# Kernel tuning notes

Measured on AMD Instinct MI355X. Metric: run time of the kernel, lower is better.

Reference implementation:

```python
import jax, jax.numpy as jnp
import numpy as np

B, N, D, C, H = 32, 36, 2048, 4, 512  # batch, regions, feat dim, coord dim, fusion hidden


def setup_inputs() -> dict:
    key = jax.random.key(0)
    ks = jax.random.split(key, 8)
    w = lambda k, sh: jax.random.normal(k, sh, dtype=jnp.float32) * 0.02
    return {
        "mm": jax.random.normal(ks[0], (B, N, D), dtype=jnp.float32),
        "coords": jax.random.uniform(ks[1], (B, N, C), dtype=jnp.float32),
        # MLB fusion params for coords: z = (x@W_cl * y@W_cr) @ W_cout
        "W_cl": w(ks[2], (C, H)),
        "W_cr": w(ks[3], (C, H)),
        "W_cout": w(ks[4], (H, D)),
        # MLB fusion params for features
        "W_fl": w(ks[5], (D, H)),
        "W_fr": w(ks[6], (D, H)),
        "W_fout": w(ks[7], (H, D)),
    }


def reference(mm, coords, W_cl, W_cr, W_cout, W_fl, W_fr, W_fout):
    # Project once per region (avoids projecting inside the N*N expand).
    cl = coords @ W_cl            # [B,N,H]
    cr = coords @ W_cr            # [B,N,H]
    fl = mm @ W_fl                # [B,N,H]
    fr = mm @ W_fr                # [B,N,H]
    # All-pairs bilinear fusion: Rij = f_coord(c_i, c_j) + f_feat(m_i, m_j)
    pair_c = cl[:, :, None, :] * cr[:, None, :, :]   # [B,N,N,H]
    pair_f = fl[:, :, None, :] * fr[:, None, :, :]   # [B,N,N,H]
    Rij = (jnp.einsum('bijh,hd->bijd', pair_c, W_cout)
           + jnp.einsum('bijh,hd->bijd', pair_f, W_fout))  # [B,N,N,D]
    # agg['type'] == 'max': reduce over the right (j) region axis
    mm_new = Rij.max(axis=2)      # [B,N,D]
    # residual
    return mm_new + mm
```

## Files before the change

kernel.cpp:

```cpp
#include <hip/hip_runtime.h>


typedef __attribute__((ext_vector_type(8))) short short8;
typedef __attribute__((ext_vector_type(4))) short short4v;
typedef __attribute__((ext_vector_type(4))) float f32x4;

__device__ __forceinline__ float bf2f(unsigned short h) {
  return __uint_as_float(((unsigned int)h) << 16);
}
__device__ __forceinline__ unsigned short f2bf(float f) {
  unsigned int u = __float_as_uint(f);
  u += 0x7FFFu + ((u >> 16) & 1u);
  return (unsigned short)(u >> 16);
}
__device__ __forceinline__ void gl2lds16(const void* g, void* l) {
  __builtin_amdgcn_global_load_lds(
      (const __attribute__((address_space(1))) unsigned int*)g,
      (__attribute__((address_space(3))) unsigned int*)l, 16, 0, 0);
}

__global__ __launch_bounds__(256) void k_prep(
    const float* __restrict__ coords, const float* __restrict__ Wcl,
    const float* __restrict__ Wcr, const float* __restrict__ mm,
    const float* __restrict__ Wcout, const float* __restrict__ Wfout,
    const float* __restrict__ Wfl, const float* __restrict__ Wfr,
    unsigned short* __restrict__ Lw, unsigned short* __restrict__ Rw,
    unsigned short* __restrict__ mmb, unsigned short* __restrict__ WS,
    unsigned short* __restrict__ WS2) {
  const int bid = blockIdx.x;
  if (bid < 2304) {
    int idx = bid * 256 + threadIdx.x;
    int row = idx >> 9, h = idx & 511;
    const float* c = coords + row * 4;
    float a0 = c[0], a1 = c[1], a2 = c[2], a3 = c[3];
    float vl = a0 * Wcl[h] + a1 * Wcl[512 + h] + a2 * Wcl[1024 + h] + a3 * Wcl[1536 + h];
    float vr = a0 * Wcr[h] + a1 * Wcr[512 + h] + a2 * Wcr[1024 + h] + a3 * Wcr[1536 + h];
    Lw[(size_t)row * 1024 + h] = f2bf(vl);
    Rw[(size_t)row * 1024 + h] = f2bf(vr);
    float4 m4 = *(const float4*)(mm + (size_t)row * 2048 + h * 4);
    short4v o;
    o[0] = (short)f2bf(m4.x); o[1] = (short)f2bf(m4.y);
    o[2] = (short)f2bf(m4.z); o[3] = (short)f2bf(m4.w);
    *(short4v*)(mmb + (size_t)row * 2048 + h * 4) = o;
  } else {
    int gi = (bid - 2304) * 256 + threadIdx.x;
    if (gi < 262144) {
      int n = gi & 15, qv = (gi >> 4) & 3, kc = (gi >> 6) & 31, g2 = gi >> 11;
      int d = g2 * 16 + n;
      int kbase = kc * 32 + qv * 8;
      const float* src = (kbase < 512) ? (Wcout + (size_t)kbase * 2048 + d)
                                       : (Wfout + (size_t)(kbase - 512) * 2048 + d);
      short8 o;
#pragma unroll
      for (int e = 0; e < 8; ++e) o[e] = (short)f2bf(src[(size_t)e * 2048]);
      *(short8*)(WS + (size_t)gi * 8) = o;
    } else {
      int gj = gi - 262144;
      int n = gj & 15, qv = (gj >> 4) & 3, kc = (gj >> 6) & 63, cg = gj >> 12;
      int col = cg * 16 + n;
      int dbase = kc * 32 + qv * 8;
      const float* src = (col < 512) ? (Wfl + (size_t)dbase * 512 + col)
                                     : (Wfr + (size_t)dbase * 512 + (col - 512));
      short8 o;
#pragma unroll
      for (int e = 0; e < 8; ++e) o[e] = (short)f2bf(src[(size_t)e * 512]);
      *(short8*)(WS2 + (size_t)gj * 8) = o;
    }
  }
}

__global__ __launch_bounds__(256) void k_proj_feat(
    const unsigned short* __restrict__ mmb, const unsigned short* __restrict__ WS2,
    unsigned short* __restrict__ Lw, unsigned short* __restrict__ Rw) {
  const int tid = threadIdx.x;
  const int lane = tid & 63, w = tid >> 6;
  const int n = lane & 15, q = lane >> 4;
  const int m0 = blockIdx.y * 16;
  const int cg = blockIdx.x * 4 + w;
  const int c0 = cg * 16;

  f32x4 acc = {0.f, 0.f, 0.f, 0.f};
#pragma unroll 4
  for (int kc = 0; kc < 64; ++kc) {
    short8 a = *(const short8*)(mmb + (size_t)(m0 + n) * 2048 + kc * 32 + q * 8);
    short8 b = *(const short8*)(WS2 + (size_t)(cg * 64 + kc) * 512 + lane * 8);
    acc = __builtin_amdgcn_mfma_f32_16x16x32_bf16(a, b, acc, 0, 0, 0);
  }
#pragma unroll
  for (int e = 0; e < 4; ++e) {
    int row = m0 + q * 4 + e;
    int col = c0 + n;
    unsigned short v = f2bf(acc[e]);
    if (col < 512) Lw[(size_t)row * 1024 + 512 + col] = v;
    else           Rw[(size_t)row * 1024 + col] = v;
  }
}

__global__ __launch_bounds__(256) void k_prod(
    const unsigned short* __restrict__ Lw, const unsigned short* __restrict__ Rw,
    unsigned short* __restrict__ Pf) {
  int idx = blockIdx.x * 256 + threadIdx.x;
  int lane = idx & 63;
  int gran = idx >> 6;
  int qg = gran / 288;
  int rem = gran - qg * 288;
  int kc = rem / 9;
  int t = rem - kc * 9;
  int n = lane & 15, q = lane >> 4;
  int k0 = kc * 32 + q * 8;
  int b = qg / 9;
  int g, j;
  if (t < 8) { g = qg * 4 + (t >> 1); j = (t & 1) * 16 + n; }
  else       { g = qg * 4 + (n >> 2); j = 32 + (n & 3); }
  short8 cl8 = *(const short8*)(Lw + (size_t)g * 1024 + k0);
  short8 cr8 = *(const short8*)(Rw + (size_t)(b * 36 + j) * 1024 + k0);
  short8 p;
#pragma unroll
  for (int e = 0; e < 8; ++e)
    p[e] = (short)f2bf(bf2f((unsigned short)cl8[e]) * bf2f((unsigned short)cr8[e]));
  *(short8*)(Pf + (size_t)idx * 8) = p;
}

__global__ __launch_bounds__(512, 2) void k_pairwise(
    const unsigned short* __restrict__ Pf, const unsigned short* __restrict__ WS,
    const float* __restrict__ mm, float* __restrict__ out) {
  __shared__ __align__(16) unsigned short lB[2][9 * 512];

  const int tid = threadIdx.x;
  const int lane = tid & 63, w = tid >> 6;
  const int n = lane & 15, q = lane >> 4;
  const int bx = blockIdx.x;
  const int dt = bx & 7, qg = bx >> 3;
  const int g0 = qg * 4;

  f32x4 acc[9][2];
#pragma unroll
  for (int t = 0; t < 9; ++t)
#pragma unroll
    for (int r = 0; r < 2; ++r) acc[t][r] = (f32x4){0.f, 0.f, 0.f, 0.f};

  const unsigned short* Abase = WS + ((size_t)(dt * 16 + w * 2) * 32) * 512 + lane * 8;
  const unsigned short* Bbase = Pf + (size_t)qg * 32 * 9 * 512;

  short8 aR[2], aN[2];
  gl2lds16(Bbase + (size_t)w * 512 + lane * 8, &lB[0][w * 512]);
  if (w == 0) gl2lds16(Bbase + (size_t)8 * 512 + lane * 8, &lB[0][8 * 512]);
  aR[0] = *(const short8*)(Abase);
  aR[1] = *(const short8*)(Abase + 32 * 512);
  __syncthreads();

#pragma unroll 2
  for (int kc = 0; kc < 32; ++kc) {
    const int buf = kc & 1;
    if (kc < 31) {
      const unsigned short* bn = Bbase + (size_t)((kc + 1) * 9) * 512 + lane * 8;
      gl2lds16(bn + (size_t)w * 512, &lB[buf ^ 1][w * 512]);
      if (w == 0) gl2lds16(bn + (size_t)8 * 512, &lB[buf ^ 1][8 * 512]);
      aN[0] = *(const short8*)(Abase + (size_t)(kc + 1) * 512);
      aN[1] = *(const short8*)(Abase + (size_t)(32 + kc + 1) * 512);
    }
    short8 bb[9];
#pragma unroll
    for (int t = 0; t < 9; ++t)
      bb[t] = *(const short8*)(&lB[buf][t * 512 + lane * 8]);
#pragma unroll
    for (int t = 0; t < 9; ++t) {
      acc[t][0] = __builtin_amdgcn_mfma_f32_16x16x32_bf16(aR[0], bb[t], acc[t][0], 0, 0, 0);
      acc[t][1] = __builtin_amdgcn_mfma_f32_16x16x32_bf16(aR[1], bb[t], acc[t][1], 0, 0, 0);
    }
    __syncthreads();
    aR[0] = aN[0];
    aR[1] = aN[1];
  }

#pragma unroll
  for (int r = 0; r < 2; ++r) {
#pragma unroll
    for (int e = 0; e < 4; ++e) {
      float vs = acc[8][r][e];
#pragma unroll
      for (int ii = 0; ii < 4; ++ii) {
        float v = fmaxf(acc[ii * 2][r][e], acc[ii * 2 + 1][r][e]);
        v = fmaxf(v, ((n >> 2) == ii) ? vs : -1e30f);
#pragma unroll
        for (int s = 1; s < 16; s <<= 1) v = fmaxf(v, __shfl_xor(v, s, 64));
        if (n == 0) {
          int d = dt * 256 + w * 32 + r * 16 + q * 4 + e;
          size_t o = (size_t)(g0 + ii) * 2048 + d;
          out[o] = v + mm[o];
        }
      }
    }
  }
}

extern "C" void kernel_launch(void* const* d_in, const int* in_sizes, int n_in,
                              void* d_out, int out_size, void* d_ws, size_t ws_size,
                              hipStream_t stream) {
  const float* mm     = (const float*)d_in[0];
  const float* coords = (const float*)d_in[1];
  const float* Wcl    = (const float*)d_in[2];
  const float* Wcr    = (const float*)d_in[3];
  const float* Wcout  = (const float*)d_in[4];
  const float* Wfl    = (const float*)d_in[5];
  const float* Wfr    = (const float*)d_in[6];
  const float* Wfout  = (const float*)d_in[7];
  float* out = (float*)d_out;

  unsigned short* Lw  = (unsigned short*)d_ws;
  unsigned short* Rw  = Lw + 1152 * 1024;
  unsigned short* WS  = Rw + 1152 * 1024;
  unsigned short* WS2 = WS + (size_t)262144 * 8;
  unsigned short* mmb = WS2 + (size_t)262144 * 8;
  unsigned short* Pf  = mmb + (size_t)1152 * 2048;

  k_prep<<<2304 + 2048, 256, 0, stream>>>(coords, Wcl, Wcr, mm, Wcout, Wfout,
                                          Wfl, Wfr, Lw, Rw, mmb, WS, WS2);
  k_proj_feat<<<dim3(16, 72), 256, 0, stream>>>(mmb, WS2, Lw, Rw);
  k_prod<<<20736, 256, 0, stream>>>(Lw, Rw, Pf);
  k_pairwise<<<2304, 512, 0, stream>>>(Pf, WS, mm, out);
}
```

Before: 338.7 us.

## Fuse pairwise product formation into the MFMA kernel, dropping the Pf buffer

Removes the separate k_prod kernel that materialized the bf16 pairwise products into a large global buffer. k_pairwise now loads Lw/Rw rows per k-chunk into registers, multiplies them and writes the products into the LDS double buffer one stage ahead. This replaces global_load_lds copies. It avoids a large global write and the repeated reads across the eight d-tiles, at the cost of recomputing the products per d-tile and adding VALU work and register pressure inside the main loop.

```diff
diff --git a/kernel.cpp b/kernel.cpp
--- a/kernel.cpp
+++ b/kernel.cpp
@@ -12,11 +12,6 @@
   unsigned int u = __float_as_uint(f);
   u += 0x7FFFu + ((u >> 16) & 1u);
   return (unsigned short)(u >> 16);
-}
-__device__ __forceinline__ void gl2lds16(const void* g, void* l) {
-  __builtin_amdgcn_global_load_lds(
-      (const __attribute__((address_space(1))) unsigned int*)g,
-      (__attribute__((address_space(3))) unsigned int*)l, 16, 0, 0);
 }
 
 __global__ __launch_bounds__(256) void k_prep(
@@ -96,34 +91,10 @@
   }
 }
 
-__global__ __launch_bounds__(256) void k_prod(
+__global__ __launch_bounds__(512, 2) void k_pairwise(
     const unsigned short* __restrict__ Lw, const unsigned short* __restrict__ Rw,
-    unsigned short* __restrict__ Pf) {
-  int idx = blockIdx.x * 256 + threadIdx.x;
-  int lane = idx & 63;
-  int gran = idx >> 6;
-  int qg = gran / 288;
-  int rem = gran - qg * 288;
-  int kc = rem / 9;
-  int t = rem - kc * 9;
-  int n = lane & 15, q = lane >> 4;
-  int k0 = kc * 32 + q * 8;
-  int b = qg / 9;
-  int g, j;
-  if (t < 8) { g = qg * 4 + (t >> 1); j = (t & 1) * 16 + n; }
-  else       { g = qg * 4 + (n >> 2); j = 32 + (n & 3); }
-  short8 cl8 = *(const short8*)(Lw + (size_t)g * 1024 + k0);
-  short8 cr8 = *(const short8*)(Rw + (size_t)(b * 36 + j) * 1024 + k0);
-  short8 p;
-#pragma unroll
-  for (int e = 0; e < 8; ++e)
-    p[e] = (short)f2bf(bf2f((unsigned short)cl8[e]) * bf2f((unsigned short)cr8[e]));
-  *(short8*)(Pf + (size_t)idx * 8) = p;
-}
-
-__global__ __launch_bounds__(512, 2) void k_pairwise(
-    const unsigned short* __restrict__ Pf, const unsigned short* __restrict__ WS,
-    const float* __restrict__ mm, float* __restrict__ out) {
+    const unsigned short* __restrict__ WS, const float* __restrict__ mm,
+    float* __restrict__ out) {
   __shared__ __align__(16) unsigned short lB[2][9 * 512];
 
   const int tid = threadIdx.x;
@@ -132,6 +103,48 @@
   const int bx = blockIdx.x;
   const int dt = bx & 7, qg = bx >> 3;
   const int g0 = qg * 4;
+  const int b = qg / 9;
+
+  const int tA = tid >> 6, lsA = tid & 63, nA = lsA & 15, qA = lsA >> 4;
+  const int gA = g0 + (tA >> 1);
+  const int jA = (tA & 1) * 16 + nA;
+  const unsigned short* clA = Lw + (size_t)gA * 1024 + qA * 8;
+  const unsigned short* crA = Rw + (size_t)(b * 36 + jA) * 1024 + qA * 8;
+  const int offA = tA * 512 + lsA * 8;
+  const bool hasB = (tid < 64);
+  const int nB = tid & 15, qB = (tid >> 4) & 3;
+  const int gB = g0 + (nB >> 2);
+  const int jB = 32 + (nB & 3);
+  const unsigned short* clB = Lw + (size_t)gB * 1024 + qB * 8;
+  const unsigned short* crB = Rw + (size_t)(b * 36 + jB) * 1024 + qB * 8;
+  const int offB = 8 * 512 + tid * 8;
+
+  short8 sclA, scrA, sclB, scrB;
+#define SLOAD(kc_)                                                   \
+  do {                                                               \
+    sclA = *(const short8*)(clA + (kc_) * 32);                       \
+    scrA = *(const short8*)(crA + (kc_) * 32);                       \
+    if (hasB) {                                                      \
+      sclB = *(const short8*)(clB + (kc_) * 32);                     \
+      scrB = *(const short8*)(crB + (kc_) * 32);                     \
+    }                                                                \
+  } while (0)
+
+#define SFIN(buf_)                                                   \
+  do {                                                               \
+    short8 p;                                                        \
+    _Pragma("unroll") for (int e = 0; e < 8; ++e)                    \
+        p[e] = (short)f2bf(bf2f((unsigned short)sclA[e]) *           \
+                           bf2f((unsigned short)scrA[e]));           \
+    *(short8*)(&lB[buf_][offA]) = p;                                 \
+    if (hasB) {                                                      \
+      short8 pb;                                                     \
+      _Pragma("unroll") for (int e = 0; e < 8; ++e)                  \
+          pb[e] = (short)f2bf(bf2f((unsigned short)sclB[e]) *        \
+                              bf2f((unsigned short)scrB[e]));        \
+      *(short8*)(&lB[buf_][offB]) = pb;                              \
+    }                                                                \
+  } while (0)
 
   f32x4 acc[9][2];
 #pragma unroll
@@ -140,11 +153,10 @@
     for (int r = 0; r < 2; ++r) acc[t][r] = (f32x4){0.f, 0.f, 0.f, 0.f};
 
   const unsigned short* Abase = WS + ((size_t)(dt * 16 + w * 2) * 32) * 512 + lane * 8;
-  const unsigned short* Bbase = Pf + (size_t)qg * 32 * 9 * 512;
-
   short8 aR[2], aN[2];
-  gl2lds16(Bbase + (size_t)w * 512 + lane * 8, &lB[0][w * 512]);
-  if (w == 0) gl2lds16(Bbase + (size_t)8 * 512 + lane * 8, &lB[0][8 * 512]);
+
+  SLOAD(0);
+  SFIN(0);
   aR[0] = *(const short8*)(Abase);
   aR[1] = *(const short8*)(Abase + 32 * 512);
   __syncthreads();
@@ -153,9 +165,7 @@
   for (int kc = 0; kc < 32; ++kc) {
     const int buf = kc & 1;
     if (kc < 31) {
-      const unsigned short* bn = Bbase + (size_t)((kc + 1) * 9) * 512 + lane * 8;
-      gl2lds16(bn + (size_t)w * 512, &lB[buf ^ 1][w * 512]);
-      if (w == 0) gl2lds16(bn + (size_t)8 * 512, &lB[buf ^ 1][8 * 512]);
+      SLOAD(kc + 1);
       aN[0] = *(const short8*)(Abase + (size_t)(kc + 1) * 512);
       aN[1] = *(const short8*)(Abase + (size_t)(32 + kc + 1) * 512);
     }
@@ -168,10 +178,13 @@
       acc[t][0] = __builtin_amdgcn_mfma_f32_16x16x32_bf16(aR[0], bb[t], acc[t][0], 0, 0, 0);
       acc[t][1] = __builtin_amdgcn_mfma_f32_16x16x32_bf16(aR[1], bb[t], acc[t][1], 0, 0, 0);
     }
+    if (kc < 31) SFIN(buf ^ 1);
     __syncthreads();
     aR[0] = aN[0];
     aR[1] = aN[1];
   }
+#undef SLOAD
+#undef SFIN
 
 #pragma unroll
   for (int r = 0; r < 2; ++r) {
@@ -212,11 +225,9 @@
   unsigned short* WS  = Rw + 1152 * 1024;
   unsigned short* WS2 = WS + (size_t)262144 * 8;
   unsigned short* mmb = WS2 + (size_t)262144 * 8;
-  unsigned short* Pf  = mmb + (size_t)1152 * 2048;
 
   k_prep<<<2304 + 2048, 256, 0, stream>>>(coords, Wcl, Wcr, mm, Wcout, Wfout,
                                           Wfl, Wfr, Lw, Rw, mmb, WS, WS2);
   k_proj_feat<<<dim3(16, 72), 256, 0, stream>>>(mmb, WS2, Lw, Rw);
-  k_prod<<<20736, 256, 0, stream>>>(Lw, Rw, Pf);
-  k_pairwise<<<2304, 512, 0, stream>>>(Pf, WS, mm, out);
-}
+  k_pairwise<<<2304, 512, 0, stream>>>(Lw, Rw, WS, mm, out);
+}
```

New measurement: 442.6 us. 1.31x slower.

## Halve pairwise block to 4 waves, each computing 4 D-tiles, reorder grid dt-major

Applied to the files above, without the earlier changes.

The pairwise GEMM block shrinks from 8 to 4 waves, and each wave now accumulates 4 output 16-row tiles instead of 2. This doubles register-level reuse of each LDS B fragment per wave and halves the per-block LDS load work per MFMA. The block index mapping is swapped so consecutive blocks share the same weight slice dt while varying qg, which changes L2 locality for the weight operand. Accumulator register pressure doubles (36 f32x4 tiles), and the unroll-2 pragma is dropped, which may reduce occupancy or cause spills.

```diff
diff --git a/kernel.cpp b/kernel.cpp
--- a/kernel.cpp
+++ b/kernel.cpp
@@ -121,7 +121,7 @@
   *(short8*)(Pf + (size_t)idx * 8) = p;
 }
 
-__global__ __launch_bounds__(512, 2) void k_pairwise(
+__global__ __launch_bounds__(256, 2) void k_pairwise(
     const unsigned short* __restrict__ Pf, const unsigned short* __restrict__ WS,
     const float* __restrict__ mm, float* __restrict__ out) {
   __shared__ __align__(16) unsigned short lB[2][9 * 512];
@@ -130,51 +130,54 @@
   const int lane = tid & 63, w = tid >> 6;
   const int n = lane & 15, q = lane >> 4;
   const int bx = blockIdx.x;
-  const int dt = bx & 7, qg = bx >> 3;
+  const int dt = bx / 288, qg = bx % 288;
   const int g0 = qg * 4;
 
-  f32x4 acc[9][2];
+  f32x4 acc[9][4];
 #pragma unroll
   for (int t = 0; t < 9; ++t)
 #pragma unroll
-    for (int r = 0; r < 2; ++r) acc[t][r] = (f32x4){0.f, 0.f, 0.f, 0.f};
-
-  const unsigned short* Abase = WS + ((size_t)(dt * 16 + w * 2) * 32) * 512 + lane * 8;
+    for (int r = 0; r < 4; ++r) acc[t][r] = (f32x4){0.f, 0.f, 0.f, 0.f};
+
+  const unsigned short* Abase = WS + (size_t)(dt * 16 + w * 4) * 32 * 512 + lane * 8;
   const unsigned short* Bbase = Pf + (size_t)qg * 32 * 9 * 512;
 
-  short8 aR[2], aN[2];
+  short8 aR[4], aN[4];
   gl2lds16(Bbase + (size_t)w * 512 + lane * 8, &lB[0][w * 512]);
+  gl2lds16(Bbase + (size_t)(4 + w) * 512 + lane * 8, &lB[0][(4 + w) * 512]);
   if (w == 0) gl2lds16(Bbase + (size_t)8 * 512 + lane * 8, &lB[0][8 * 512]);
-  aR[0] = *(const short8*)(Abase);
-  aR[1] = *(const short8*)(Abase + 32 * 512);
+#pragma unroll
+  for (int r = 0; r < 4; ++r)
+    aR[r] = *(const short8*)(Abase + (size_t)r * 32 * 512);
   __syncthreads();
 
-#pragma unroll 2
   for (int kc = 0; kc < 32; ++kc) {
     const int buf = kc & 1;
     if (kc < 31) {
       const unsigned short* bn = Bbase + (size_t)((kc + 1) * 9) * 512 + lane * 8;
       gl2lds16(bn + (size_t)w * 512, &lB[buf ^ 1][w * 512]);
+      gl2lds16(bn + (size_t)(4 + w) * 512, &lB[buf ^ 1][(4 + w) * 512]);
       if (w == 0) gl2lds16(bn + (size_t)8 * 512, &lB[buf ^ 1][8 * 512]);
-      aN[0] = *(const short8*)(Abase + (size_t)(kc + 1) * 512);
-      aN[1] = *(const short8*)(Abase + (size_t)(32 + kc + 1) * 512);
+#pragma unroll
+      for (int r = 0; r < 4; ++r)
+        aN[r] = *(const short8*)(Abase + (size_t)(r * 32 + kc + 1) * 512);
     }
     short8 bb[9];
 #pragma unroll
     for (int t = 0; t < 9; ++t)
       bb[t] = *(const short8*)(&lB[buf][t * 512 + lane * 8]);
 #pragma unroll
-    for (int t = 0; t < 9; ++t) {
-      acc[t][0] = __builtin_amdgcn_mfma_f32_16x16x32_bf16(aR[0], bb[t], acc[t][0], 0, 0, 0);
-      acc[t][1] = __builtin_amdgcn_mfma_f32_16x16x32_bf16(aR[1], bb[t], acc[t][1], 0, 0, 0);
-    }
+    for (int t = 0; t < 9; ++t)
+#pragma unroll
+      for (int r = 0; r < 4; ++r)
+        acc[t][r] = __builtin_amdgcn_mfma_f32_16x16x32_bf16(aR[r], bb[t], acc[t][r], 0, 0, 0);
     __syncthreads();
-    aR[0] = aN[0];
-    aR[1] = aN[1];
-  }
-
-#pragma unroll
-  for (int r = 0; r < 2; ++r) {
+#pragma unroll
+    for (int r = 0; r < 4; ++r) aR[r] = aN[r];
+  }
+
+#pragma unroll
+  for (int r = 0; r < 4; ++r) {
 #pragma unroll
     for (int e = 0; e < 4; ++e) {
       float vs = acc[8][r][e];
@@ -185,7 +188,7 @@
 #pragma unroll
         for (int s = 1; s < 16; s <<= 1) v = fmaxf(v, __shfl_xor(v, s, 64));
         if (n == 0) {
-          int d = dt * 256 + w * 32 + r * 16 + q * 4 + e;
+          int d = dt * 256 + (w * 4 + r) * 16 + q * 4 + e;
           size_t o = (size_t)(g0 + ii) * 2048 + d;
           out[o] = v + mm[o];
         }
@@ -218,5 +221,5 @@
                                           Wfl, Wfr, Lw, Rw, mmb, WS, WS2);
   k_proj_feat<<<dim3(16, 72), 256, 0, stream>>>(mmb, WS2, Lw, Rw);
   k_prod<<<20736, 256, 0, stream>>>(Lw, Rw, Pf);
-  k_pairwise<<<2304, 512, 0, stream>>>(Pf, WS, mm, out);
-}
+  k_pairwise<<<2304, 256, 0, stream>>>(Pf, WS, mm, out);
+}
```

Measured after the change: 378.2 us. +11.7%, slower.
